# Kernel optimization log

Hardware: AMD Instinct MI355X
Metric: run time of the kernel (lower is better)

Reference implementation:

```python
import jax, jax.numpy as jnp
import numpy as np

EMBED_DIM = 1024
NUM_HEADS = 16
HEAD_DIM = EMBED_DIM // NUM_HEADS
SCALE = HEAD_DIM ** -0.5
EPS = 1e-5


def layer_norm(x, gamma, beta):
    mu = jnp.mean(x, axis=-1, keepdims=True)
    var = jnp.var(x, axis=-1, keepdims=True)
    return (x - mu) * jax.lax.rsqrt(var + EPS) * gamma + beta


def setup_inputs() -> dict:
    key = jax.random.key(0)
    ks = jax.random.split(key, 12)
    d = EMBED_DIM
    xav = (6.0 / (d + d)) ** 0.5
    x = jax.random.normal(ks[0], (4, 1024, d), dtype=jnp.float32)
    Wq = jax.random.uniform(ks[1], (d, d), jnp.float32, -xav, xav)
    Wk = jax.random.uniform(ks[2], (d, d), jnp.float32, -xav, xav)
    Wv = jax.random.uniform(ks[3], (d, d), jnp.float32, -xav, xav)
    Wo = jax.random.uniform(ks[4], (d, d), jnp.float32, -xav, xav)
    bq = jnp.zeros((d,), jnp.float32)
    bk = jnp.zeros((d,), jnp.float32)
    bv = jnp.zeros((d,), jnp.float32)
    bo = jnp.zeros((d,), jnp.float32)
    ones = jnp.ones((d,), jnp.float32)
    zeros = jnp.zeros((d,), jnp.float32)
    return {
        "x": x,
        "Wq": Wq, "bq": bq, "Wk": Wk, "bk": bk, "Wv": Wv, "bv": bv,
        "Wo": Wo, "bo": bo,
        "qn_g": ones, "qn_b": zeros,
        "kn_g": ones, "kn_b": zeros,
        "vn_g": ones, "vn_b": zeros,
        "on_g": ones, "on_b": zeros,
    }


def reference(x, Wq, bq, Wk, bk, Wv, bv, Wo, bo,
              qn_g, qn_b, kn_g, kn_b, vn_g, vn_b, on_g, on_b):
    B, S, D = x.shape
    H, Hd = NUM_HEADS, HEAD_DIM
    # projections (nn.Linear: x @ W.T + b) followed by LayerNorm
    Q = layer_norm(x @ Wq.T + bq, qn_g, qn_b) * SCALE
    K = layer_norm(x @ Wk.T + bk, kn_g, kn_b)
    V = layer_norm(x @ Wv.T + bv, vn_g, vn_b)
    Q = Q.reshape(B, S, H, Hd).transpose(0, 2, 1, 3)  # [B,H,S,Hd]
    K = K.reshape(B, S, H, Hd).transpose(0, 2, 1, 3)
    V = V.reshape(B, S, H, Hd).transpose(0, 2, 1, 3)
    scores = jnp.einsum('bhqd,bhkd->bhqk', Q, K)
    scores = jnp.clip(scores, -10.0, 10.0)
    attn = jax.nn.softmax(scores, axis=-1)  # dropout = identity at eval
    out = jnp.einsum('bhqk,bhkd->bhqd', attn, V)
    out = out.transpose(0, 2, 1, 3).reshape(B, S, D)
    out = out @ Wo.T + bo
    return layer_norm(out, on_g, on_b)
```

## Files before the change

kernel.cpp:

```cpp
#include <hip/hip_runtime.h>
#include <stdint.h>
#include <stddef.h>

typedef unsigned short u16;
typedef __bf16 bf16x8 __attribute__((ext_vector_type(8)));
typedef float f32x4 __attribute__((ext_vector_type(4)));
typedef float f32x16 __attribute__((ext_vector_type(16)));
typedef u16 u16x8 __attribute__((ext_vector_type(8)));
typedef unsigned uint32x2 __attribute__((ext_vector_type(2)));

#define SEQ    1024
#define DEMB   1024
#define MROWS  4096
#define NHEAD  16
#define HD     64
#define QSCALE 0.125f
#define LN_EPS 1e-5f

static __device__ __forceinline__ u16 f2bf(float f) {
  union { float f; unsigned u; } c; c.f = f;
  unsigned r = c.u + 0x7FFFu + ((c.u >> 16) & 1u);
  return (u16)(r >> 16);
}
static __device__ __forceinline__ float bf2f(unsigned h) {
  union { unsigned u; float f; } c; c.u = h << 16; return c.f;
}
static __device__ __forceinline__ unsigned pack2bf(float a, float b) {
  union { __bf16 h; u16 u; } x, y; x.h = (__bf16)a; y.h = (__bf16)b;
  return (unsigned)x.u | ((unsigned)y.u << 16);
}

static __device__ __forceinline__ void gload16(const void* g, void* l) {
  __builtin_amdgcn_global_load_lds((const __attribute__((address_space(1))) void*)g,
                                   (__attribute__((address_space(3))) void*)l, 16, 0, 0);
}

__global__ void cvt_kernel(const float* __restrict__ x,
                           const float* __restrict__ wq, const float* __restrict__ wk,
                           const float* __restrict__ wv, const float* __restrict__ wo,
                           u16* __restrict__ xb, u16* __restrict__ wb) {
  size_t e = ((size_t)blockIdx.x * blockDim.x + threadIdx.x) * 8;
  const float* src; u16* dst; size_t off;
  if (e < (size_t)MROWS * DEMB) { src = x; dst = xb; off = e; }
  else {
    size_t we = e - (size_t)MROWS * DEMB;
    int plane = (int)(we >> 20);
    src = (plane == 0) ? wq : (plane == 1) ? wk : (plane == 2) ? wv : wo;
    dst = wb + ((size_t)plane << 20);
    off = we & ((1u << 20) - 1);
  }
  float4 a = *(const float4*)(src + off);
  float4 b = *(const float4*)(src + off + 4);
  u16 o[8] = { f2bf(a.x), f2bf(a.y), f2bf(a.z), f2bf(a.w),
               f2bf(b.x), f2bf(b.y), f2bf(b.z), f2bf(b.w) };
  uint4 pk;
  pk.x = (unsigned)o[0] | ((unsigned)o[1] << 16);
  pk.y = (unsigned)o[2] | ((unsigned)o[3] << 16);
  pk.z = (unsigned)o[4] | ((unsigned)o[5] << 16);
  pk.w = (unsigned)o[6] | ((unsigned)o[7] << 16);
  *(uint4*)(dst + off) = pk;
}

__global__ __launch_bounds__(256)
void gemm_bt(const u16* __restrict__ A, const u16* __restrict__ B0,
             const u16* __restrict__ B1, const u16* __restrict__ B2,
             u16* __restrict__ C, int M, int N, int K) {
  __shared__ u16 lA[128 * 32];
  __shared__ u16 lB[128 * 32];
  const u16* Bp = (blockIdx.z == 0) ? B0 : (blockIdx.z == 1) ? B1 : B2;
  u16* Cp = C + (size_t)blockIdx.z * ((size_t)M * N);
  const int tid = threadIdx.x;
  const int w = tid >> 6, l = tid & 63;
  const int lr = l & 15, lg = l >> 4;
  const int m0 = blockIdx.x * 128, n0 = blockIdx.y * 128;
  const int wm = (w & 1) * 64, wn = (w >> 1) * 64;
  f32x4 acc[4][4] = {};
  const int cid0 = w * 64 + l;
  const int cid1 = 256 + w * 64 + l;
  const int rowA0 = cid0 >> 2, kc0 = (cid0 & 3) * 8;
  const int rowA1 = cid1 >> 2, kc1 = (cid1 & 3) * 8;
  for (int kt = 0; kt < K; kt += 32) {
    __syncthreads();
    gload16(A  + (size_t)(m0 + rowA0) * K + kt + kc0, lA + (size_t)(w * 64) * 8);
    gload16(A  + (size_t)(m0 + rowA1) * K + kt + kc1, lA + (size_t)(256 + w * 64) * 8);
    gload16(Bp + (size_t)(n0 + rowA0) * K + kt + kc0, lB + (size_t)(w * 64) * 8);
    gload16(Bp + (size_t)(n0 + rowA1) * K + kt + kc1, lB + (size_t)(256 + w * 64) * 8);
    __syncthreads();
    bf16x8 af[4], bfg[4];
#pragma unroll
    for (int mb = 0; mb < 4; ++mb) {
      union { u16x8 u; bf16x8 v; } cv;
      cv.u = *(const u16x8*)(lA + (wm + mb * 16 + lr) * 32 + lg * 8);
      af[mb] = cv.v;
    }
#pragma unroll
    for (int nb = 0; nb < 4; ++nb) {
      union { u16x8 u; bf16x8 v; } cv;
      cv.u = *(const u16x8*)(lB + (wn + nb * 16 + lr) * 32 + lg * 8);
      bfg[nb] = cv.v;
    }
#pragma unroll
    for (int mb = 0; mb < 4; ++mb)
#pragma unroll
      for (int nb = 0; nb < 4; ++nb)
        acc[mb][nb] = __builtin_amdgcn_mfma_f32_16x16x32_bf16(af[mb], bfg[nb], acc[mb][nb], 0, 0, 0);
  }
#pragma unroll
  for (int mb = 0; mb < 4; ++mb)
#pragma unroll
    for (int nb = 0; nb < 4; ++nb)
#pragma unroll
      for (int r = 0; r < 4; ++r) {
        int row = m0 + wm + mb * 16 + lg * 4 + r;
        int col = n0 + wn + nb * 16 + lr;
        Cp[(size_t)row * N + col] = f2bf(acc[mb][nb][r]);
      }
}

static __device__ __forceinline__ void block_reduce2(float& s1, float& s2, float* red) {
#pragma unroll
  for (int o = 32; o > 0; o >>= 1) { s1 += __shfl_xor(s1, o); s2 += __shfl_xor(s2, o); }
  int w = threadIdx.x >> 6, l = threadIdx.x & 63;
  if (l == 0) { red[w * 2] = s1; red[w * 2 + 1] = s2; }
  __syncthreads();
  s1 = red[0] + red[2] + red[4] + red[6];
  s2 = red[1] + red[3] + red[5] + red[7];
}

__global__ void ln_qkv_kernel(const u16* __restrict__ projb,
                              const float* __restrict__ bq, const float* __restrict__ bk,
                              const float* __restrict__ bv,
                              const float* __restrict__ qg, const float* __restrict__ qb,
                              const float* __restrict__ kg, const float* __restrict__ kb,
                              const float* __restrict__ vg, const float* __restrict__ vb,
                              u16* __restrict__ Qh, u16* __restrict__ Kh, u16* __restrict__ Vh) {
  __shared__ float red[8];
  const int row = blockIdx.x & (MROWS - 1);
  const int plane = blockIdx.x >> 12;
  const float* bias; const float* gam; const float* bet; u16* op; float scl;
  if (plane == 0)      { bias = bq; gam = qg; bet = qb; op = Qh; scl = QSCALE; }
  else if (plane == 1) { bias = bk; gam = kg; bet = kb; op = Kh; scl = 1.f; }
  else                 { bias = bv; gam = vg; bet = vb; op = Vh; scl = 1.f; }
  const u16* src = projb + ((size_t)plane * MROWS + row) * DEMB;
  const int t = threadIdx.x;
  uint2 pv = *(const uint2*)(src + t * 4);
  float4 v;
  v.x = bf2f(pv.x & 0xffffu); v.y = bf2f(pv.x >> 16);
  v.z = bf2f(pv.y & 0xffffu); v.w = bf2f(pv.y >> 16);
  float4 bz = *(const float4*)(bias + t * 4);
  v.x += bz.x; v.y += bz.y; v.z += bz.z; v.w += bz.w;
  float s1 = v.x + v.y + v.z + v.w;
  float s2 = v.x * v.x + v.y * v.y + v.z * v.z + v.w * v.w;
  block_reduce2(s1, s2, red);
  const float mean = s1 * (1.f / DEMB);
  const float var = s2 * (1.f / DEMB) - mean * mean;
  const float rstd = rsqrtf(var + LN_EPS);
  float4 gg = *(const float4*)(gam + t * 4);
  float4 bb = *(const float4*)(bet + t * 4);
  u16 o0 = f2bf(((v.x - mean) * rstd * gg.x + bb.x) * scl);
  u16 o1 = f2bf(((v.y - mean) * rstd * gg.y + bb.y) * scl);
  u16 o2 = f2bf(((v.z - mean) * rstd * gg.z + bb.z) * scl);
  u16 o3 = f2bf(((v.w - mean) * rstd * gg.w + bb.w) * scl);
  const int b = row >> 10, s = row & (SEQ - 1);
  const int h = t >> 4;
  u16* dst = op + ((size_t)(b * NHEAD + h) * SEQ + s) * HD + (t & 15) * 4;
  uint2 pk;
  pk.x = (unsigned)o0 | ((unsigned)o1 << 16);
  pk.y = (unsigned)o2 | ((unsigned)o3 << 16);
  *(uint2*)dst = pk;
}

__global__ __launch_bounds__(256)
void vtr_kernel(const u16* __restrict__ Vtmp, u16* __restrict__ VT) {
  __shared__ u16 t[64][72];
  const int stile = blockIdx.x & 15, bh = blockIdx.x >> 4;
  const u16* src = Vtmp + ((size_t)bh * SEQ + stile * 64) * HD;
  const int tid = threadIdx.x;
  {
    const int c0 = tid * 2;
    const int r = c0 >> 3, c = c0 & 7;
    uint4 v0 = *(const uint4*)(src + (size_t)r * HD + c * 8);
    uint4 v1 = *(const uint4*)(src + (size_t)r * HD + (c + 1) * 8);
    *(uint4*)&t[r][c * 8] = v0;
    *(uint4*)&t[r][(c + 1) * 8] = v1;
  }
  __syncthreads();
  const int d = tid >> 2, sc = tid & 3;
  u16 buf[16];
#pragma unroll
  for (int j = 0; j < 16; ++j) buf[j] = t[sc * 16 + j][d];
  u16* dst = VT + ((size_t)bh * HD + d) * SEQ + stile * 64 + sc * 16;
  *(uint4*)(dst)     = *(uint4*)&buf[0];
  *(uint4*)(dst + 8) = *(uint4*)&buf[8];
}

__global__ __launch_bounds__(128)
void attn_kernel(const u16* __restrict__ Qh, const u16* __restrict__ Kh,
                 const u16* __restrict__ VT, u16* __restrict__ AO) {
  __shared__ float oL[32][64];
  __shared__ float rsL[32];
  const int bid = blockIdx.x;
  const int wg = (bid & 7) * 256 + (bid >> 3);
  const int qt = wg & 31, bh = wg >> 5;
  const int b = bh >> 4, h = bh & 15;
  const u16* Qp = Qh + (size_t)bh * SEQ * HD;
  const u16* Kp = Kh + (size_t)bh * SEQ * HD;
  const u16* Vp = VT + (size_t)bh * HD * SEQ;
  const int tid = threadIdx.x, w = tid >> 6, l = tid & 63;
  const int q = l & 31, hi = l >> 5;
  bf16x8 qf[4];
#pragma unroll
  for (int dt = 0; dt < 4; ++dt) {
    union { u16x8 u; bf16x8 v; } cv;
    cv.u = *(const u16x8*)(Qp + (size_t)(qt * 32 + q) * HD + dt * 16 + hi * 8);
    qf[dt] = cv.v;
  }
  f32x16 o0 = {}, o1 = {};
  float rs = 0.f;
  const int kbase = w * (SEQ / 2);
  for (int t = 0; t < 8; ++t) {
    const int k0 = kbase + t * 64;
    unsigned W[2][8];
#pragma unroll
    for (int kc = 0; kc < 2; ++kc) {
      f32x16 sc = {};
#pragma unroll
      for (int dt = 0; dt < 4; ++dt) {
        union { u16x8 u; bf16x8 v; } cv;
        cv.u = *(const u16x8*)(Kp + (size_t)(k0 + kc * 32 + q) * HD + dt * 16 + hi * 8);
        sc = __builtin_amdgcn_mfma_f32_32x32x16_bf16(cv.v, qf[dt], sc, 0, 0, 0);
      }
      float pv[16];
#pragma unroll
      for (int r = 0; r < 16; ++r) {
        float xx = fminf(10.f, fmaxf(-10.f, sc[r]));
        float p = exp2f(xx * 1.4426950408889634f);
        rs += p;
        pv[r] = p;
      }
#pragma unroll
      for (int i = 0; i < 8; ++i)
        W[kc][i] = pack2bf(pv[2 * i], pv[2 * i + 1]);
    }
#pragma unroll
    for (int kt = 0; kt < 4; ++kt) {
      const int kcx = kt >> 1, ktl = kt & 1;
      uint32x2 s0 = __builtin_amdgcn_permlane32_swap(W[kcx][4 * ktl + 0], W[kcx][4 * ktl + 2], false, false);
      uint32x2 s1 = __builtin_amdgcn_permlane32_swap(W[kcx][4 * ktl + 1], W[kcx][4 * ktl + 3], false, false);
      union { unsigned u[4]; bf16x8 v; } pa;
      pa.u[0] = s0[0]; pa.u[1] = s1[0]; pa.u[2] = s0[1]; pa.u[3] = s1[1];
      {
        union { u16x8 u; bf16x8 v; } v0, v1;
        v0.u = *(const u16x8*)(Vp + (size_t)(0 * 32 + q) * SEQ + k0 + kt * 16 + hi * 8);
        v1.u = *(const u16x8*)(Vp + (size_t)(1 * 32 + q) * SEQ + k0 + kt * 16 + hi * 8);
        o0 = __builtin_amdgcn_mfma_f32_32x32x16_bf16(pa.v, v0.v, o0, 0, 0, 0);
        o1 = __builtin_amdgcn_mfma_f32_32x32x16_bf16(pa.v, v1.v, o1, 0, 0, 0);
      }
    }
  }
  rs += __shfl_xor(rs, 32);
  if (w == 1) {
#pragma unroll
    for (int r = 0; r < 16; ++r) {
      const int row = (r & 3) + 8 * (r >> 2) + 4 * hi;
      oL[row][q]      = o0[r];
      oL[row][32 + q] = o1[r];
    }
    if (hi == 0) rsL[q] = rs;
  }
  __syncthreads();
  if (w == 0) {
    const float inv_q = 1.f / (rs + rsL[q]);
#pragma unroll
    for (int r = 0; r < 16; ++r) {
      const int row = (r & 3) + 8 * (r >> 2) + 4 * hi;
      const float invr = __shfl(inv_q, row);
      const int srow = qt * 32 + row;
      const size_t base = ((size_t)b * SEQ + srow) * DEMB + h * HD;
      AO[base + q]      = f2bf((o0[r] + oL[row][q]) * invr);
      AO[base + 32 + q] = f2bf((o1[r] + oL[row][32 + q]) * invr);
    }
  }
}

__global__ void ln_out_kernel(const u16* __restrict__ src0, const float* __restrict__ bo,
                              const float* __restrict__ og, const float* __restrict__ ob,
                              float* __restrict__ out) {
  __shared__ float red[8];
  const int row = blockIdx.x;
  const u16* src = src0 + (size_t)row * DEMB;
  const int t = threadIdx.x;
  uint2 pv = *(const uint2*)(src + t * 4);
  float4 v;
  v.x = bf2f(pv.x & 0xffffu); v.y = bf2f(pv.x >> 16);
  v.z = bf2f(pv.y & 0xffffu); v.w = bf2f(pv.y >> 16);
  float4 bz = *(const float4*)(bo + t * 4);
  v.x += bz.x; v.y += bz.y; v.z += bz.z; v.w += bz.w;
  float s1 = v.x + v.y + v.z + v.w;
  float s2 = v.x * v.x + v.y * v.y + v.z * v.z + v.w * v.w;
  block_reduce2(s1, s2, red);
  const float mean = s1 * (1.f / DEMB);
  const float var = s2 * (1.f / DEMB) - mean * mean;
  const float rstd = rsqrtf(var + LN_EPS);
  float4 gg = *(const float4*)(og + t * 4);
  float4 bb = *(const float4*)(ob + t * 4);
  float4 r;
  r.x = (v.x - mean) * rstd * gg.x + bb.x;
  r.y = (v.y - mean) * rstd * gg.y + bb.y;
  r.z = (v.z - mean) * rstd * gg.z + bb.z;
  r.w = (v.w - mean) * rstd * gg.w + bb.w;
  *(float4*)(out + (size_t)row * DEMB + t * 4) = r;
}

extern "C" void kernel_launch(void* const* d_in, const int* in_sizes, int n_in,
                              void* d_out, int out_size, void* d_ws, size_t ws_size,
                              hipStream_t stream) {
  (void)in_sizes; (void)n_in; (void)out_size; (void)ws_size;
  const float* x  = (const float*)d_in[0];
  const float* Wq = (const float*)d_in[1];
  const float* bq = (const float*)d_in[2];
  const float* Wk = (const float*)d_in[3];
  const float* bk = (const float*)d_in[4];
  const float* Wv = (const float*)d_in[5];
  const float* bv = (const float*)d_in[6];
  const float* Wo = (const float*)d_in[7];
  const float* bo = (const float*)d_in[8];
  const float* qg = (const float*)d_in[9];
  const float* qb = (const float*)d_in[10];
  const float* kg = (const float*)d_in[11];
  const float* kb = (const float*)d_in[12];
  const float* vg = (const float*)d_in[13];
  const float* vb = (const float*)d_in[14];
  const float* og = (const float*)d_in[15];
  const float* ob = (const float*)d_in[16];

  char* ws = (char*)d_ws;
  u16* xb    = (u16*)(ws);
  u16* wb    = (u16*)(ws + ((size_t)8  << 20));
  u16* projb = (u16*)(ws + ((size_t)16 << 20));
  u16* Qh    = (u16*)(ws + ((size_t)40 << 20));
  u16* Kh    = (u16*)(ws + ((size_t)48 << 20));
  u16* VT    = (u16*)(ws + ((size_t)56 << 20));
  u16* Vtmp  = xb;
  u16* AOp   = xb;
  u16* oprojb = projb;

  cvt_kernel<<<4096, 256, 0, stream>>>(x, Wq, Wk, Wv, Wo, xb, wb);

  dim3 gqkv(32, 8, 3);
  gemm_bt<<<gqkv, 256, 0, stream>>>(xb, wb, wb + (1u << 20), wb + (2u << 20),
                                    projb, MROWS, DEMB, DEMB);

  ln_qkv_kernel<<<3 * MROWS, 256, 0, stream>>>(projb, bq, bk, bv,
                                               qg, qb, kg, kb, vg, vb,
                                               Qh, Kh, Vtmp);

  vtr_kernel<<<1024, 256, 0, stream>>>(Vtmp, VT);

  attn_kernel<<<2048, 128, 0, stream>>>(Qh, Kh, VT, AOp);

  dim3 go(32, 8, 1);
  gemm_bt<<<go, 256, 0, stream>>>(AOp, wb + (3u << 20), wb + (3u << 20), wb + (3u << 20),
                                  oprojb, MROWS, DEMB, DEMB);

  ln_out_kernel<<<MROWS, 256, 0, stream>>>(oprojb, bo, og, ob, (float*)d_out);
}
```

Measured before the change: 256.8 us.

## Stage K/V tiles in swizzled LDS shared by four query-tile waves

The attention kernel now assigns 128 query rows per block, one 32-row tile per wave, and each wave covers the full key range, so the split-K reduction through LDS goes away. Each 64-key tile of K and V^T is loaded cooperatively into XOR-swizzled shared memory and read by all four waves, replacing per-wave direct global loads. This cuts redundant global and L2 traffic for K/V. The cost is two barriers per tile with no double buffering, and a grid of 512 blocks instead of 2048.

```diff
diff --git a/kernel.cpp b/kernel.cpp
--- a/kernel.cpp
+++ b/kernel.cpp
@@ -194,32 +194,43 @@
   *(uint4*)(dst + 8) = *(uint4*)&buf[8];
 }
 
-__global__ __launch_bounds__(128)
+__global__ __launch_bounds__(256)
 void attn_kernel(const u16* __restrict__ Qh, const u16* __restrict__ Kh,
                  const u16* __restrict__ VT, u16* __restrict__ AO) {
-  __shared__ float oL[32][64];
-  __shared__ float rsL[32];
+  __shared__ u16 lK[64 * 64];
+  __shared__ u16 lV[64 * 64];
   const int bid = blockIdx.x;
-  const int wg = (bid & 7) * 256 + (bid >> 3);
-  const int qt = wg & 31, bh = wg >> 5;
+  const int wg = (bid & 7) * 64 + (bid >> 3);
+  const int qt = wg & 7, bh = wg >> 3;
   const int b = bh >> 4, h = bh & 15;
   const u16* Qp = Qh + (size_t)bh * SEQ * HD;
   const u16* Kp = Kh + (size_t)bh * SEQ * HD;
   const u16* Vp = VT + (size_t)bh * HD * SEQ;
   const int tid = threadIdx.x, w = tid >> 6, l = tid & 63;
   const int q = l & 31, hi = l >> 5;
+  const int c0 = tid, c1 = 256 + tid;
+  const int lc0 = c0 ^ ((c0 >> 3) & 7), lc1 = c1 ^ ((c1 >> 3) & 7);
+  const int r0 = lc0 >> 3, cc0 = (lc0 & 7) * 8;
+  const int r1 = lc1 >> 3, cc1 = (lc1 & 7) * 8;
   bf16x8 qf[4];
+  const int qrow = qt * 128 + w * 32 + q;
 #pragma unroll
   for (int dt = 0; dt < 4; ++dt) {
     union { u16x8 u; bf16x8 v; } cv;
-    cv.u = *(const u16x8*)(Qp + (size_t)(qt * 32 + q) * HD + dt * 16 + hi * 8);
+    cv.u = *(const u16x8*)(Qp + (size_t)qrow * HD + dt * 16 + hi * 8);
     qf[dt] = cv.v;
   }
   f32x16 o0 = {}, o1 = {};
   float rs = 0.f;
-  const int kbase = w * (SEQ / 2);
-  for (int t = 0; t < 8; ++t) {
-    const int k0 = kbase + t * 64;
+  const int swz = (q & 7) * 8;
+  for (int t = 0; t < 16; ++t) {
+    const int k0 = t * 64;
+    __syncthreads();
+    gload16(Kp + (size_t)(k0 + r0) * HD + cc0, lK + (size_t)(w * 64) * 8);
+    gload16(Kp + (size_t)(k0 + r1) * HD + cc1, lK + (size_t)(256 + w * 64) * 8);
+    gload16(Vp + (size_t)r0 * SEQ + k0 + cc0, lV + (size_t)(w * 64) * 8);
+    gload16(Vp + (size_t)r1 * SEQ + k0 + cc1, lV + (size_t)(256 + w * 64) * 8);
+    __syncthreads();
     unsigned W[2][8];
 #pragma unroll
     for (int kc = 0; kc < 2; ++kc) {
@@ -227,7 +238,7 @@
 #pragma unroll
       for (int dt = 0; dt < 4; ++dt) {
         union { u16x8 u; bf16x8 v; } cv;
-        cv.u = *(const u16x8*)(Kp + (size_t)(k0 + kc * 32 + q) * HD + dt * 16 + hi * 8);
+        cv.u = *(const u16x8*)(lK + (kc * 32 + q) * 64 + ((dt * 16 + hi * 8) ^ swz));
         sc = __builtin_amdgcn_mfma_f32_32x32x16_bf16(cv.v, qf[dt], sc, 0, 0, 0);
       }
       float pv[16];
@@ -249,37 +260,23 @@
       uint32x2 s1 = __builtin_amdgcn_permlane32_swap(W[kcx][4 * ktl + 1], W[kcx][4 * ktl + 3], false, false);
       union { unsigned u[4]; bf16x8 v; } pa;
       pa.u[0] = s0[0]; pa.u[1] = s1[0]; pa.u[2] = s0[1]; pa.u[3] = s1[1];
-      {
-        union { u16x8 u; bf16x8 v; } v0, v1;
-        v0.u = *(const u16x8*)(Vp + (size_t)(0 * 32 + q) * SEQ + k0 + kt * 16 + hi * 8);
-        v1.u = *(const u16x8*)(Vp + (size_t)(1 * 32 + q) * SEQ + k0 + kt * 16 + hi * 8);
-        o0 = __builtin_amdgcn_mfma_f32_32x32x16_bf16(pa.v, v0.v, o0, 0, 0, 0);
-        o1 = __builtin_amdgcn_mfma_f32_32x32x16_bf16(pa.v, v1.v, o1, 0, 0, 0);
-      }
+      union { u16x8 u; bf16x8 v; } v0, v1;
+      v0.u = *(const u16x8*)(lV + (q) * 64 + ((kt * 16 + hi * 8) ^ swz));
+      v1.u = *(const u16x8*)(lV + (32 + q) * 64 + ((kt * 16 + hi * 8) ^ swz));
+      o0 = __builtin_amdgcn_mfma_f32_32x32x16_bf16(pa.v, v0.v, o0, 0, 0, 0);
+      o1 = __builtin_amdgcn_mfma_f32_32x32x16_bf16(pa.v, v1.v, o1, 0, 0, 0);
     }
   }
   rs += __shfl_xor(rs, 32);
-  if (w == 1) {
-#pragma unroll
-    for (int r = 0; r < 16; ++r) {
-      const int row = (r & 3) + 8 * (r >> 2) + 4 * hi;
-      oL[row][q]      = o0[r];
-      oL[row][32 + q] = o1[r];
-    }
-    if (hi == 0) rsL[q] = rs;
-  }
-  __syncthreads();
-  if (w == 0) {
-    const float inv_q = 1.f / (rs + rsL[q]);
-#pragma unroll
-    for (int r = 0; r < 16; ++r) {
-      const int row = (r & 3) + 8 * (r >> 2) + 4 * hi;
-      const float invr = __shfl(inv_q, row);
-      const int srow = qt * 32 + row;
-      const size_t base = ((size_t)b * SEQ + srow) * DEMB + h * HD;
-      AO[base + q]      = f2bf((o0[r] + oL[row][q]) * invr);
-      AO[base + 32 + q] = f2bf((o1[r] + oL[row][32 + q]) * invr);
-    }
+  const float inv_q = 1.f / rs;
+#pragma unroll
+  for (int r = 0; r < 16; ++r) {
+    const int row = (r & 3) + 8 * (r >> 2) + 4 * hi;
+    const float invr = __shfl(inv_q, row);
+    const int srow = qt * 128 + w * 32 + row;
+    const size_t base = ((size_t)b * SEQ + srow) * DEMB + h * HD;
+    AO[base + q]      = f2bf(o0[r] * invr);
+    AO[base + 32 + q] = f2bf(o1[r] * invr);
   }
 }
 
@@ -357,7 +354,7 @@
 
   vtr_kernel<<<1024, 256, 0, stream>>>(Vtmp, VT);
 
-  attn_kernel<<<2048, 128, 0, stream>>>(Qh, Kh, VT, AOp);
+  attn_kernel<<<512, 256, 0, stream>>>(Qh, Kh, VT, AOp);
 
   dim3 go(32, 8, 1);
   gemm_bt<<<go, 256, 0, stream>>>(AOp, wb + (3u << 20), wb + (3u << 20), wb + (3u << 20),
```

Result: faster. 232.0 us (-9.7%).
